# Kernel optimization log

Measured on AMD Instinct MI355X. Metric: run time of the kernel, lower is better.

## Reference

```python
import jax, jax.numpy as jnp
import numpy as np

NUM_ACTIONS = 8
SHIFT_BINS = jnp.asarray([-16., -8., -4., 0., 4., 8., 16.], dtype=jnp.float32)
NUM_SHIFT_BINS = 7

B, L, D = 32, 4096, 1024


def setup_inputs() -> dict:
    key = jax.random.key(0)
    ks = jax.random.split(key, 8)
    s = lambda fan_in: 1.0 / np.sqrt(fan_in)
    return {
        "embeddings": jax.random.normal(ks[0], (B, L, D), dtype=jnp.float32),
        "actions": jax.random.randint(ks[1], (B, L), 0, NUM_ACTIONS),
        "mask": jnp.ones((B, L), dtype=bool),
        "sw1": jax.random.uniform(ks[2], (D, 128), minval=-s(D), maxval=s(D)),
        "sb1": jnp.zeros((128,), dtype=jnp.float32),
        "sw2": jax.random.uniform(ks[3], (128, 2 * NUM_SHIFT_BINS), minval=-s(128), maxval=s(128)),
        "sb2": jnp.zeros((2 * NUM_SHIFT_BINS,), dtype=jnp.float32),
        "ew1": jax.random.uniform(ks[4], (D, 64), minval=-s(D), maxval=s(D)),
        "eb1": jnp.zeros((64,), dtype=jnp.float32),
        "ew2": jax.random.uniform(ks[5], (64, 3), minval=-s(64), maxval=s(64)),
        "eb2": jnp.zeros((3,), dtype=jnp.float32),
    }


def reference(embeddings, actions, mask, sw1, sb1, sw2, sb2, ew1, eb1, ew2, eb2):
    # one-hot segment reduce: [B,L,A] masked one-hot, single pass over L via einsum
    onehot = jax.nn.one_hot(actions, NUM_ACTIONS, dtype=embeddings.dtype)  # [B,L,A]
    onehot = onehot * mask[..., None].astype(embeddings.dtype)
    counts = onehot.sum(axis=1)  # [B,A]
    summed = jnp.einsum("bla,bld->bad", onehot, embeddings)  # [B,A,D]
    feats = summed / jnp.clip(counts, 1.0, None)[..., None]  # mean per action

    shift_logits = jnp.maximum(feats @ sw1 + sb1, 0.0) @ sw2 + sb2  # [B,A,14]
    dx_logits = shift_logits[..., :NUM_SHIFT_BINS]
    dy_logits = shift_logits[..., NUM_SHIFT_BINS:]
    shift_dx = (jax.nn.softmax(dx_logits, axis=-1) * SHIFT_BINS).sum(-1)
    shift_dy = (jax.nn.softmax(dy_logits, axis=-1) * SHIFT_BINS).sum(-1)
    shift = jnp.stack([shift_dx, shift_dy], axis=-1)  # [B,A,2]

    effects = jnp.maximum(feats @ ew1 + eb1, 0.0) @ ew2 + eb2  # [B,A,3]
    seen = (counts > 0).astype(embeddings.dtype)  # [B,A]

    return (
        shift * seen[..., None],
        dx_logits,
        dy_logits,
        jax.nn.sigmoid(effects[..., 0]) * seen,
        jax.nn.sigmoid(effects[..., 1]) * seen,
        effects[..., 2] * seen,
    )
```

## Files before the change

### kernel.cpp

```cpp
#include <hip/hip_runtime.h>
#include <math.h>

#define B_ 32
#define L_ 4096
#define D_ 1024
#define A_ 8
#define CHUNK 256
#define NSB 7

__global__ __launch_bounds__(256) void k_accum(
    const float* __restrict__ emb, const int* __restrict__ actions,
    const int* __restrict__ mask,
    float* __restrict__ sums , float* __restrict__ counts )
{
  const int chunks_per_b = L_ / CHUNK;
  const int b  = blockIdx.x / chunks_per_b;
  const int l0 = (blockIdx.x % chunks_per_b) * CHUNK;
  const int t  = threadIdx.x;

  __shared__ int s_act[CHUNK];
  for (int i = t; i < CHUNK; i += 256) {
    const int idx = b * L_ + l0 + i;
    const int a = actions[idx];
    s_act[i] = (mask[idx] != 0) ? a : -1;
  }
  __syncthreads();

  if (t < A_) {
    int cnt = 0;
    for (int i = 0; i < CHUNK; ++i) cnt += (s_act[i] == t) ? 1 : 0;
    if (cnt) atomicAdd(&counts[b * A_ + t], (float)cnt);
  }

  float4 acc[A_];
#pragma unroll
  for (int j = 0; j < A_; ++j) acc[j] = make_float4(0.f, 0.f, 0.f, 0.f);

  const float4* __restrict__ row =
      (const float4*)(emb + (size_t)(b * L_ + l0) * D_);

#define ADD4(J, V) \
  acc[J].x += (V).x; acc[J].y += (V).y; acc[J].z += (V).z; acc[J].w += (V).w

#pragma unroll 1
  for (int i = 0; i < CHUNK; i += 8) {
    float4 v[8];
#pragma unroll
    for (int u = 0; u < 8; ++u) v[u] = row[(size_t)(i + u) * (D_ / 4) + t];
#pragma unroll
    for (int u = 0; u < 8; ++u) {
      const int a = __builtin_amdgcn_readfirstlane(s_act[i + u]);
      switch (a) {
        case 0: ADD4(0, v[u]); break;
        case 1: ADD4(1, v[u]); break;
        case 2: ADD4(2, v[u]); break;
        case 3: ADD4(3, v[u]); break;
        case 4: ADD4(4, v[u]); break;
        case 5: ADD4(5, v[u]); break;
        case 6: ADD4(6, v[u]); break;
        case 7: ADD4(7, v[u]); break;
        default: break;
      }
    }
  }
#undef ADD4

  float* __restrict__ dst = sums + (size_t)b * A_ * D_;
#pragma unroll
  for (int j = 0; j < A_; ++j) {
    float* p = dst + j * D_ + 4 * t;
    atomicAdd(p + 0, acc[j].x);
    atomicAdd(p + 1, acc[j].y);
    atomicAdd(p + 2, acc[j].z);
    atomicAdd(p + 3, acc[j].w);
  }
}

__global__ __launch_bounds__(256) void k_head(
    const float* __restrict__ sums, const float* __restrict__ counts,
    const float* __restrict__ sw1, const float* __restrict__ sb1,
    const float* __restrict__ sw2, const float* __restrict__ sb2,
    const float* __restrict__ ew1, const float* __restrict__ eb1,
    const float* __restrict__ ew2, const float* __restrict__ eb2,
    float* __restrict__ out)
{
  const int ba = blockIdx.x;
  const int t  = threadIdx.x;

  __shared__ float s_feat[D_];
  __shared__ float s_h1[128];
  __shared__ float s_he[64];
  __shared__ float s_logits[2 * NSB];
  __shared__ float s_eff[3];

  const float cnt = counts[ba];
  const float inv = 1.0f / fmaxf(cnt, 1.0f);
  for (int d = t; d < D_; d += 256) s_feat[d] = sums[(size_t)ba * D_ + d] * inv;
  __syncthreads();

  if (t < 128) {
    float acc = sb1[t];
#pragma unroll 4
    for (int d = 0; d < D_; ++d) acc += s_feat[d] * sw1[d * 128 + t];
    s_h1[t] = fmaxf(acc, 0.f);
  } else if (t < 192) {
    const int j = t - 128;
    float acc = eb1[j];
#pragma unroll 4
    for (int d = 0; d < D_; ++d) acc += s_feat[d] * ew1[d * 64 + j];
    s_he[j] = fmaxf(acc, 0.f);
  }
  __syncthreads();

  if (t < 2 * NSB) {
    float acc = sb2[t];
#pragma unroll 4
    for (int k = 0; k < 128; ++k) acc += s_h1[k] * sw2[k * (2 * NSB) + t];
    s_logits[t] = acc;
  } else if (t < 2 * NSB + 3) {
    const int j = t - 2 * NSB;
    float acc = eb2[j];
#pragma unroll 4
    for (int k = 0; k < 64; ++k) acc += s_he[k] * ew2[k * 3 + j];
    s_eff[j] = acc;
  }
  __syncthreads();

  const float seen = (cnt > 0.f) ? 1.f : 0.f;

  float* __restrict__ out0 = out;
  float* __restrict__ out1 = out + 512;
  float* __restrict__ out2 = out + 2304;
  float* __restrict__ out3 = out + 4096;
  float* __restrict__ out4 = out + 4352;
  float* __restrict__ out5 = out + 4608;

  if (t < NSB) {
    out1[ba * NSB + t] = s_logits[t];
    out2[ba * NSB + t] = s_logits[NSB + t];
  }

  if (t == 0) {
    const float bins[NSB] = {-16.f, -8.f, -4.f, 0.f, 4.f, 8.f, 16.f};
    float dxy[2];
#pragma unroll
    for (int h = 0; h < 2; ++h) {
      const float* lg = &s_logits[h * NSB];
      float m = lg[0];
      for (int i = 1; i < NSB; ++i) m = fmaxf(m, lg[i]);
      float s = 0.f, acc = 0.f;
      for (int i = 0; i < NSB; ++i) {
        const float e = expf(lg[i] - m);
        s += e;
        acc += e * bins[i];
      }
      dxy[h] = acc / s;
    }
    out0[ba * 2 + 0] = dxy[0] * seen;
    out0[ba * 2 + 1] = dxy[1] * seen;
    out3[ba] = (1.f / (1.f + expf(-s_eff[0]))) * seen;
    out4[ba] = (1.f / (1.f + expf(-s_eff[1]))) * seen;
    out5[ba] = s_eff[2] * seen;
  }
}

extern "C" void kernel_launch(void* const* d_in, const int* in_sizes, int n_in,
                              void* d_out, int out_size, void* d_ws, size_t ws_size,
                              hipStream_t stream) {
  const float* emb     = (const float*)d_in[0];
  const int*   actions = (const int*)d_in[1];
  const int*   mask    = (const int*)d_in[2];
  const float* sw1 = (const float*)d_in[3];
  const float* sb1 = (const float*)d_in[4];
  const float* sw2 = (const float*)d_in[5];
  const float* sb2 = (const float*)d_in[6];
  const float* ew1 = (const float*)d_in[7];
  const float* eb1 = (const float*)d_in[8];
  const float* ew2 = (const float*)d_in[9];
  const float* eb2 = (const float*)d_in[10];
  float* out = (float*)d_out;

  float* sums   = (float*)d_ws;
  float* counts = sums + B_ * A_ * D_;

  hipMemsetAsync(d_ws, 0, (size_t)(B_ * A_ * D_ + B_ * A_) * sizeof(float),
                 stream);

  hipLaunchKernelGGL(k_accum, dim3(B_ * (L_ / CHUNK)), dim3(256), 0, stream,
                     emb, actions, mask, sums, counts);
  hipLaunchKernelGGL(k_head, dim3(B_ * A_), dim3(256), 0, stream,
                     sums, counts, sw1, sb1, sw2, sb2, ew1, eb1, ew2, eb2, out);
}
```

Measured before the change: 845.3 us.

## Replace atomic accumulation with per-chunk partial sums reduced in head kernel

The accumulation kernel now writes per-chunk partial sums and counts to distinct workspace slots with plain float4 stores, instead of issuing atomicAdds into a zeroed buffer. This removes the memset launch and the atomic traffic. The head kernel reduces the 16 partials itself and splits the first-layer matvecs across all 256 threads using partial dot products. It uses a larger workspace (16x the sums) and adds read traffic in the head kernel.

```diff
diff --git a/kernel.cpp b/kernel.cpp
--- a/kernel.cpp
+++ b/kernel.cpp
@@ -6,16 +6,18 @@
 #define D_ 1024
 #define A_ 8
 #define CHUNK 256
+#define NCH (L_ / CHUNK)
 #define NSB 7
 
 __global__ __launch_bounds__(256) void k_accum(
     const float* __restrict__ emb, const int* __restrict__ actions,
     const int* __restrict__ mask,
-    float* __restrict__ sums , float* __restrict__ counts )
+    float* __restrict__ psums ,
+    float* __restrict__ pcnt  )
 {
-  const int chunks_per_b = L_ / CHUNK;
-  const int b  = blockIdx.x / chunks_per_b;
-  const int l0 = (blockIdx.x % chunks_per_b) * CHUNK;
+  const int b  = blockIdx.x / NCH;
+  const int c  = blockIdx.x % NCH;
+  const int l0 = c * CHUNK;
   const int t  = threadIdx.x;
 
   __shared__ int s_act[CHUNK];
@@ -29,7 +31,7 @@
   if (t < A_) {
     int cnt = 0;
     for (int i = 0; i < CHUNK; ++i) cnt += (s_act[i] == t) ? 1 : 0;
-    if (cnt) atomicAdd(&counts[b * A_ + t], (float)cnt);
+    pcnt[(b * A_ + t) * NCH + c] = (float)cnt;
   }
 
   float4 acc[A_];
@@ -65,19 +67,16 @@
   }
 #undef ADD4
 
-  float* __restrict__ dst = sums + (size_t)b * A_ * D_;
 #pragma unroll
   for (int j = 0; j < A_; ++j) {
-    float* p = dst + j * D_ + 4 * t;
-    atomicAdd(p + 0, acc[j].x);
-    atomicAdd(p + 1, acc[j].y);
-    atomicAdd(p + 2, acc[j].z);
-    atomicAdd(p + 3, acc[j].w);
+    float4* p =
+        (float4*)(psums + ((size_t)(b * A_ + j) * NCH + c) * D_) + t;
+    *p = acc[j];
   }
 }
 
 __global__ __launch_bounds__(256) void k_head(
-    const float* __restrict__ sums, const float* __restrict__ counts,
+    const float* __restrict__ psums, const float* __restrict__ pcnt,
     const float* __restrict__ sw1, const float* __restrict__ sb1,
     const float* __restrict__ sw2, const float* __restrict__ sb2,
     const float* __restrict__ ew1, const float* __restrict__ eb1,
@@ -88,27 +87,61 @@
   const int t  = threadIdx.x;
 
   __shared__ float s_feat[D_];
+  __shared__ float s_pA[256];
+  __shared__ float s_pB[256];
   __shared__ float s_h1[128];
   __shared__ float s_he[64];
   __shared__ float s_logits[2 * NSB];
   __shared__ float s_eff[3];
-
-  const float cnt = counts[ba];
+  __shared__ float s_cnt16[NCH];
+
+  if (t < NCH) s_cnt16[t] = pcnt[ba * NCH + t];
+
+  float4 a = make_float4(0.f, 0.f, 0.f, 0.f);
+  const float4* __restrict__ ps =
+      (const float4*)(psums + (size_t)ba * NCH * D_);
+#pragma unroll
+  for (int c = 0; c < NCH; ++c) {
+    const float4 v = ps[(size_t)c * (D_ / 4) + t];
+    a.x += v.x; a.y += v.y; a.z += v.z; a.w += v.w;
+  }
+  __syncthreads();
+
+  float cnt = 0.f;
+#pragma unroll
+  for (int i = 0; i < NCH; ++i) cnt += s_cnt16[i];
   const float inv = 1.0f / fmaxf(cnt, 1.0f);
-  for (int d = t; d < D_; d += 256) s_feat[d] = sums[(size_t)ba * D_ + d] * inv;
+
+  a.x *= inv; a.y *= inv; a.z *= inv; a.w *= inv;
+  ((float4*)s_feat)[t] = a;
+  __syncthreads();
+
+  {
+    const int col = t & 127;
+    const int d0  = (t >> 7) * (D_ / 2);
+    float acc = 0.f;
+#pragma unroll 8
+    for (int d = 0; d < D_ / 2; ++d)
+      acc += s_feat[d0 + d] * sw1[(d0 + d) * 128 + col];
+    s_pA[t] = acc;
+  }
+  {
+    const int col = t & 63;
+    const int d0  = (t >> 6) * (D_ / 4);
+    float acc = 0.f;
+#pragma unroll 8
+    for (int d = 0; d < D_ / 4; ++d)
+      acc += s_feat[d0 + d] * ew1[(d0 + d) * 64 + col];
+    s_pB[t] = acc;
+  }
   __syncthreads();
 
   if (t < 128) {
-    float acc = sb1[t];
-#pragma unroll 4
-    for (int d = 0; d < D_; ++d) acc += s_feat[d] * sw1[d * 128 + t];
-    s_h1[t] = fmaxf(acc, 0.f);
+    s_h1[t] = fmaxf(s_pA[t] + s_pA[128 + t] + sb1[t], 0.f);
   } else if (t < 192) {
     const int j = t - 128;
-    float acc = eb1[j];
-#pragma unroll 4
-    for (int d = 0; d < D_; ++d) acc += s_feat[d] * ew1[d * 64 + j];
-    s_he[j] = fmaxf(acc, 0.f);
+    s_he[j] = fmaxf(s_pB[j] + s_pB[64 + j] + s_pB[128 + j] + s_pB[192 + j]
+                    + eb1[j], 0.f);
   }
   __syncthreads();
 
@@ -180,14 +213,11 @@
   const float* eb2 = (const float*)d_in[10];
   float* out = (float*)d_out;
 
-  float* sums   = (float*)d_ws;
-  float* counts = sums + B_ * A_ * D_;
-
-  hipMemsetAsync(d_ws, 0, (size_t)(B_ * A_ * D_ + B_ * A_) * sizeof(float),
-                 stream);
-
-  hipLaunchKernelGGL(k_accum, dim3(B_ * (L_ / CHUNK)), dim3(256), 0, stream,
-                     emb, actions, mask, sums, counts);
+  float* psums = (float*)d_ws;
+  float* pcnt  = psums + (size_t)B_ * A_ * NCH * D_;
+
+  hipLaunchKernelGGL(k_accum, dim3(B_ * NCH), dim3(256), 0, stream,
+                     emb, actions, mask, psums, pcnt);
   hipLaunchKernelGGL(k_head, dim3(B_ * A_), dim3(256), 0, stream,
-                     sums, counts, sw1, sb1, sw2, sb2, ew1, eb1, ew2, eb2, out);
+                     psums, pcnt, sw1, sb1, sw2, sb2, ew1, eb1, ew2, eb2, out);
 }
```

New measurement: 761.9 us. 9.9% less time.
